# Kernel optimization log

Hardware: AMD Instinct MI355X
Metric: run time of the kernel (lower is better)

Reference implementation:

```python
import jax, jax.numpy as jnp
import numpy as np

B, S, H = 2, 1024, 2048
NH, NKV, HD = 16, 4, 128           # heads, kv heads, head_dim
E, TOPK, NG, TOPKG, M = 8, 2, 4, 2, 512  # experts, top_k, n_group, topk_group, moe ffn dim
EPS = 1e-6
THETA = 10000.0
SCALE = HD ** -0.5
RSF = 1.0  # routed_scaling_factor


def rmsnorm(x, w):
    xf = x.astype(jnp.float32)
    var = jnp.mean(xf * xf, axis=-1, keepdims=True)
    return (w * (xf * jax.lax.rsqrt(var + EPS))).astype(x.dtype)


def rotate_half(x):
    x1, x2 = jnp.split(x, 2, axis=-1)
    return jnp.concatenate([-x2, x1], axis=-1)


def setup_inputs() -> dict:
    key = jax.random.key(0)
    ks = jax.random.split(key, 16)
    s = 0.02
    hidden_states = jax.random.normal(ks[0], (B, S, H), jnp.float32)
    pos = jnp.arange(S, dtype=jnp.float32)
    inv_freq = 1.0 / (THETA ** (jnp.arange(0, HD, 2, dtype=jnp.float32) / HD))
    freqs = jnp.outer(pos, inv_freq)                       # [S, HD/2]
    emb = jnp.concatenate([freqs, freqs], axis=-1)         # [S, HD]
    cos = jnp.broadcast_to(jnp.cos(emb)[None], (B, S, HD))
    sin = jnp.broadcast_to(jnp.sin(emb)[None], (B, S, HD))
    return {
        "hidden_states": hidden_states,
        "cos": cos,
        "sin": sin,
        "ln1_w": jnp.ones((H,), jnp.float32),
        "w_qkv": jax.random.normal(ks[1], ((NH + 2 * NKV) * HD, H), jnp.float32) * s,
        "q_ln_w": jnp.ones((HD,), jnp.float32),
        "k_ln_w": jnp.ones((HD,), jnp.float32),
        "w_dense": jax.random.normal(ks[2], (H, NH * HD), jnp.float32) * s,
        "ln2_w": jnp.ones((H,), jnp.float32),
        "gate_w": jax.random.normal(ks[3], (E, H), jnp.float32) * s,
        "gate_bias": jnp.zeros((E,), jnp.float32),
        "we_gate": jax.random.normal(ks[4], (E, M, H), jnp.float32) * s,
        "we_up": jax.random.normal(ks[5], (E, M, H), jnp.float32) * s,
        "we_down": jax.random.normal(ks[6], (E, H, M), jnp.float32) * s,
        "ws_gate": jax.random.normal(ks[7], (M, H), jnp.float32) * s,
        "ws_up": jax.random.normal(ks[8], (M, H), jnp.float32) * s,
        "ws_down": jax.random.normal(ks[9], (H, M), jnp.float32) * s,
    }


def reference(hidden_states, cos, sin, ln1_w, w_qkv, q_ln_w, k_ln_w, w_dense,
              ln2_w, gate_w, gate_bias, we_gate, we_up, we_down,
              ws_gate, ws_up, ws_down):
    # ---- attention block ----
    residual = hidden_states
    x = rmsnorm(hidden_states, ln1_w)
    qkv = jnp.einsum('bsh,oh->bso', x, w_qkv).reshape(B, S, NH + 2 * NKV, HD)
    q, k, v = jnp.split(qkv, [NH, NH + NKV], axis=2)
    q = q.transpose(0, 2, 1, 3)   # [B, NH,  S, HD]
    k = k.transpose(0, 2, 1, 3)   # [B, NKV, S, HD]
    v = v.transpose(0, 2, 1, 3)
    q = rmsnorm(q, q_ln_w)
    k = rmsnorm(k, k_ln_w)
    c, sn = cos[:, None], sin[:, None]  # [B,1,S,HD]
    q = q * c + rotate_half(q) * sn
    k = k * c + rotate_half(k) * sn
    n_rep = NH // NKV
    k = jnp.repeat(k, n_rep, axis=1)
    v = jnp.repeat(v, n_rep, axis=1)
    scores = jnp.einsum('bhqd,bhkd->bhqk', q, k) * SCALE
    attn = jax.nn.softmax(scores.astype(jnp.float32), axis=-1).astype(q.dtype)
    out = jnp.einsum('bhqk,bhkd->bhqd', attn, v)
    out = out.transpose(0, 2, 1, 3).reshape(B, S, NH * HD)
    attn_out = jnp.einsum('bso,ho->bsh', out, w_dense)
    hidden = residual + attn_out

    # ---- MoE block ----
    residual = hidden
    x = rmsnorm(hidden, ln2_w).reshape(B * S, H)
    T = B * S
    logits = jnp.einsum('th,eh->te', x.astype(jnp.float32), gate_w.astype(jnp.float32))
    scores = jax.nn.sigmoid(logits)
    scores_b = scores + gate_bias
    # group-limited routing: pick topk_group groups by sum of top-2 scores per group
    gsz = E // NG
    grp = scores_b.reshape(T, NG, gsz)
    top2 = jax.lax.top_k(grp, min(2, gsz))[0].sum(-1)      # [T, NG]
    _, gidx = jax.lax.top_k(top2, TOPKG)                   # [T, TOPKG]
    gmask = jnp.zeros((T, NG), scores.dtype).at[jnp.arange(T)[:, None], gidx].set(1.0)
    emask = jnp.repeat(gmask, gsz, axis=-1)                # [T, E]
    masked = jnp.where(emask > 0, scores_b, -jnp.inf)
    _, tidx = jax.lax.top_k(masked, TOPK)                  # [T, TOPK]
    tw = jnp.take_along_axis(scores, tidx, axis=-1)
    tw = tw / (tw.sum(-1, keepdims=True) + 1e-20) * RSF
    route = jnp.zeros((T, E), x.dtype).at[jnp.arange(T)[:, None], tidx].set(tw.astype(x.dtype))
    # dense all-expert compute, combined by (sparse) routing weights
    g = jnp.einsum('th,emh->tem', x, we_gate)
    u = jnp.einsum('th,emh->tem', x, we_up)
    he = jax.nn.silu(g) * u
    oe = jnp.einsum('tem,ehm->teh', he, we_down)
    moe = jnp.einsum('te,teh->th', route, oe)
    # shared expert
    sh = jnp.einsum('th,oh->to', jax.nn.silu(x @ ws_gate.T) * (x @ ws_up.T), ws_down)
    out = residual + (moe + sh).reshape(B, S, H)
    return out
```

## Files before the change

### kernel.cpp

```cpp
#include <hip/hip_runtime.h>
#include <cstdint>
#include <cstddef>

#define T_TOK 2048
#define H_DIM 2048
#define S_LEN 1024
#define HD 128
#define NH 16
#define NKV 4
#define QKV_O 3072
#define MM 512
#define EPS 1e-6f
#define ATT_SCALE 0.08838834764831845f

typedef __bf16 bf16x8 __attribute__((ext_vector_type(8)));
typedef __bf16 bf16x4 __attribute__((ext_vector_type(4)));
typedef float  f32x4  __attribute__((ext_vector_type(4)));

__device__ __forceinline__ __bf16 f2bf(float f) {
  unsigned u = __builtin_bit_cast(unsigned, f);
  u += 0x7fffu + ((u >> 16) & 1u);
  unsigned short h = (unsigned short)(u >> 16);
  return __builtin_bit_cast(__bf16, h);
}
__device__ __forceinline__ f32x4 fzero4() {
  f32x4 z; z[0] = 0.f; z[1] = 0.f; z[2] = 0.f; z[3] = 0.f; return z;
}
__device__ __forceinline__ void gld16(const __bf16* g, __bf16* l) {
  __builtin_amdgcn_global_load_lds(
      (const __attribute__((address_space(1))) unsigned int*)g,
      (__attribute__((address_space(3))) unsigned int*)l, 16, 0, 0);
}

__global__ __launch_bounds__(256) void wconv_k(
    const float* __restrict__ s0, const float* __restrict__ s1,
    __bf16* __restrict__ dst) {
  size_t e = ((size_t)blockIdx.x * 256 + threadIdx.x) * 16;
  const size_t E0 = 6291456;
  const float* src; size_t base;
  if (e < E0) { src = s0; base = 0; }
  else        { src = s1; base = E0; }
  const float4* sp = (const float4*)(src + (e - base));
  float4 f0 = sp[0], f1 = sp[1], f2 = sp[2], f3 = sp[3];
  bf16x8 o0, o1;
  o0[0] = f2bf(f0.x); o0[1] = f2bf(f0.y); o0[2] = f2bf(f0.z); o0[3] = f2bf(f0.w);
  o0[4] = f2bf(f1.x); o0[5] = f2bf(f1.y); o0[6] = f2bf(f1.z); o0[7] = f2bf(f1.w);
  o1[0] = f2bf(f2.x); o1[1] = f2bf(f2.y); o1[2] = f2bf(f2.z); o1[3] = f2bf(f2.w);
  o1[4] = f2bf(f3.x); o1[5] = f2bf(f3.y); o1[6] = f2bf(f3.z); o1[7] = f2bf(f3.w);
  *(bf16x8*)(dst + e) = o0;
  *(bf16x8*)(dst + e + 8) = o1;
}

__global__ __launch_bounds__(256) void rmsnorm_k(const float* __restrict__ X,
                                                 const float* __restrict__ W,
                                                 __bf16* __restrict__ Y) {
  int t = blockIdx.x;
  int tid = threadIdx.x, lane = tid & 63, wid = tid >> 6;
  const float4* row = (const float4*)(X + (size_t)t * H_DIM);
  float4 v0 = row[tid], v1 = row[tid + 256];
  float ss = v0.x*v0.x + v0.y*v0.y + v0.z*v0.z + v0.w*v0.w
           + v1.x*v1.x + v1.y*v1.y + v1.z*v1.z + v1.w*v1.w;
  #pragma unroll
  for (int m = 1; m <= 32; m <<= 1) ss += __shfl_xor(ss, m, 64);
  __shared__ float red[4];
  if (lane == 0) red[wid] = ss;
  __syncthreads();
  float tot = red[0] + red[1] + red[2] + red[3];
  float sc = rsqrtf(tot * (1.f / H_DIM) + EPS);
  const float4* wp = (const float4*)W;
  float4 w0 = wp[tid], w1 = wp[tid + 256];
  bf16x4 o;
  o[0] = f2bf(v0.x*w0.x*sc); o[1] = f2bf(v0.y*w0.y*sc);
  o[2] = f2bf(v0.z*w0.z*sc); o[3] = f2bf(v0.w*w0.w*sc);
  *(bf16x4*)&Y[(size_t)t*H_DIM + tid*4] = o;
  o[0] = f2bf(v1.x*w1.x*sc); o[1] = f2bf(v1.y*w1.y*sc);
  o[2] = f2bf(v1.z*w1.z*sc); o[3] = f2bf(v1.w*w1.w*sc);
  *(bf16x4*)&Y[(size_t)t*H_DIM + 1024 + tid*4] = o;
}

template<int MODE>
__global__ __launch_bounds__(256) void gemm64_nt(
    const __bf16* __restrict__ A, const __bf16* __restrict__ B,
    float* __restrict__ C, __bf16* __restrict__ OB,
    const float* __restrict__ resid, int N, int K) {
  int m0 = blockIdx.y * 64;
  int n0 = blockIdx.x * 128;
  __shared__ __bf16 sA[2][64 * 64];
  __shared__ __bf16 sB[2][128 * 64];
  int tid = threadIdx.x, lane = tid & 63, wid = tid >> 6;
  int quad = lane >> 4, l16 = lane & 15;
  int wm = wid & 1, wn = wid >> 1;

  const __bf16* gA[2]; const __bf16* gB[4];
  #pragma unroll
  for (int i = 0; i < 2; i++) {
    int p = tid + 256 * i;
    int row = p >> 3, sc = p & 7, gc = sc ^ (row & 7);
    gA[i] = A + (size_t)(m0 + row) * K + gc * 8;
  }
  #pragma unroll
  for (int i = 0; i < 4; i++) {
    int p = tid + 256 * i;
    int row = p >> 3, sc = p & 7, gc = sc ^ (row & 7);
    gB[i] = B + (size_t)(n0 + row) * K + gc * 8;
  }
  f32x4 acc[2][4];
  #pragma unroll
  for (int i = 0; i < 2; i++)
    #pragma unroll
    for (int j = 0; j < 4; j++) acc[i][j] = fzero4();

  auto stage = [&](int buf, int k0) {
    #pragma unroll
    for (int i = 0; i < 2; i++)
      gld16(gA[i] + k0, &sA[buf][(tid + 256 * i) * 8]);
    #pragma unroll
    for (int i = 0; i < 4; i++)
      gld16(gB[i] + k0, &sB[buf][(tid + 256 * i) * 8]);
  };
  stage(0, 0);
  int cur = 0;
  for (int k0 = 0; k0 < K; k0 += 64) {
    __syncthreads();
    if (k0 + 64 < K) stage(cur ^ 1, k0 + 64);
    #pragma unroll
    for (int ks = 0; ks < 64; ks += 32) {
      int cb = ks >> 3;
      bf16x8 aF[2], bF[4];
      #pragma unroll
      for (int mt = 0; mt < 2; mt++) {
        int row = wm * 32 + mt * 16 + l16;
        int pos = row * 8 + ((cb + quad) ^ (row & 7));
        aF[mt] = *(const bf16x8*)&sA[cur][pos * 8];
      }
      #pragma unroll
      for (int nt = 0; nt < 4; nt++) {
        int row = wn * 64 + nt * 16 + l16;
        int pos = row * 8 + ((cb + quad) ^ (row & 7));
        bF[nt] = *(const bf16x8*)&sB[cur][pos * 8];
      }
      #pragma unroll
      for (int mt = 0; mt < 2; mt++)
        #pragma unroll
        for (int nt = 0; nt < 4; nt++)
          acc[mt][nt] = __builtin_amdgcn_mfma_f32_16x16x32_bf16(
              aF[mt], bF[nt], acc[mt][nt], 0, 0, 0);
    }
    cur ^= 1;
  }
  #pragma unroll
  for (int mt = 0; mt < 2; mt++) {
    #pragma unroll
    for (int nt = 0; nt < 4; nt++) {
      #pragma unroll
      for (int r = 0; r < 4; r++) {
        int grow = m0 + wm*32 + mt*16 + quad*4 + r;
        int gcol = n0 + wn*64 + nt*16 + l16;
        float val = acc[mt][nt][r];
        if (MODE == 0) {
          OB[(size_t)grow * N + gcol] = f2bf(val);
        } else {
          C[(size_t)grow * H_DIM + gcol] = val + resid[(size_t)grow * H_DIM + gcol];
        }
      }
    }
  }
}

__global__ __launch_bounds__(256) void gemm_down(
    const __bf16* __restrict__ A, const float* __restrict__ B,
    const float* __restrict__ B2, __bf16* __restrict__ OB,
    const int* __restrict__ list, const signed char* __restrict__ jsl,
    const int* __restrict__ cnt) {
  int e  = blockIdx.z;
  int ne = (e == 8) ? T_TOK : cnt[e];
  int m0 = blockIdx.y * 128;
  if (m0 >= ne) return;
  int n0 = blockIdx.x * 128;
  const __bf16* Ab = A + (size_t)e * T_TOK * MM;
  const float*  Bb = (e < 8) ? B + (size_t)e * H_DIM * MM : B2;
  const int K = MM;
  __shared__ __bf16 sA[2][128 * 64];
  __shared__ __bf16 sB[2][128 * 64];
  int tid = threadIdx.x, lane = tid & 63, wid = tid >> 6;
  int quad = lane >> 4, l16 = lane & 15;
  int wm = wid & 1, wn = wid >> 1;

  const __bf16* gA[4]; const float* gB[4];
  #pragma unroll
  for (int i = 0; i < 4; i++) {
    int p = tid + 256 * i;
    int row = p >> 3, sc = p & 7, gc = sc ^ (row & 7);
    gA[i] = Ab + (size_t)(m0 + row) * K + gc * 8;
    gB[i] = Bb + (size_t)(n0 + row) * K + gc * 8;
  }
  f32x4 acc[4][4];
  #pragma unroll
  for (int i = 0; i < 4; i++)
    #pragma unroll
    for (int j = 0; j < 4; j++) acc[i][j] = fzero4();

  f32x4 br[4][2];
  auto stageA = [&](int buf, int k0) {
    #pragma unroll
    for (int i = 0; i < 4; i++)
      gld16(gA[i] + k0, &sA[buf][(tid + 256 * i) * 8]);
  };
  auto loadB = [&](int k0) {
    #pragma unroll
    for (int i = 0; i < 4; i++) {
      br[i][0] = *(const f32x4*)(gB[i] + k0);
      br[i][1] = *(const f32x4*)(gB[i] + k0 + 4);
    }
  };
  auto writeB = [&](int buf) {
    #pragma unroll
    for (int i = 0; i < 4; i++) {
      int p = tid + 256 * i;
      bf16x8 o;
      #pragma unroll
      for (int j = 0; j < 4; j++) { o[j] = f2bf(br[i][0][j]); o[j+4] = f2bf(br[i][1][j]); }
      *(bf16x8*)&sB[buf][p * 8] = o;
    }
  };
  stageA(0, 0); loadB(0); writeB(0);
  int cur = 0;
  for (int k0 = 0; k0 < K; k0 += 64) {
    __syncthreads();
    bool nxt = (k0 + 64 < K);
    if (nxt) { stageA(cur ^ 1, k0 + 64); loadB(k0 + 64); }
    #pragma unroll
    for (int ks = 0; ks < 64; ks += 32) {
      int cb = ks >> 3;
      bf16x8 aF[4], bF[4];
      #pragma unroll
      for (int mt = 0; mt < 4; mt++) {
        int row = wm * 64 + mt * 16 + l16;
        int pos = row * 8 + ((cb + quad) ^ (row & 7));
        aF[mt] = *(const bf16x8*)&sA[cur][pos * 8];
      }
      #pragma unroll
      for (int nt = 0; nt < 4; nt++) {
        int row = wn * 64 + nt * 16 + l16;
        int pos = row * 8 + ((cb + quad) ^ (row & 7));
        bF[nt] = *(const bf16x8*)&sB[cur][pos * 8];
      }
      #pragma unroll
      for (int mt = 0; mt < 4; mt++)
        #pragma unroll
        for (int nt = 0; nt < 4; nt++)
          acc[mt][nt] = __builtin_amdgcn_mfma_f32_16x16x32_bf16(
              aF[mt], bF[nt], acc[mt][nt], 0, 0, 0);
    }
    if (nxt) writeB(cur ^ 1);
    cur ^= 1;
  }
  #pragma unroll
  for (int mt = 0; mt < 4; mt++) {
    #pragma unroll
    for (int nt = 0; nt < 4; nt++) {
      #pragma unroll
      for (int r = 0; r < 4; r++) {
        int grow = m0 + wm*64 + mt*16 + quad*4 + r;
        int gcol = n0 + wn*64 + nt*16 + l16;
        if (grow < ne) {
          int tk = list[e * T_TOK + grow];
          int j  = (e == 8) ? 2 : (int)jsl[e * T_TOK + grow];
          OB[((size_t)tk * 3 + j) * H_DIM + gcol] = f2bf(acc[mt][nt][r]);
        }
      }
    }
  }
}

__global__ __launch_bounds__(256) void combine_k(const __bf16* __restrict__ buf,
                                                 float* __restrict__ out) {
  int t = blockIdx.x, tid = threadIdx.x;
  const __bf16* base = buf + (size_t)t * 3 * H_DIM;
  bf16x8 v0 = *(const bf16x8*)(base + tid * 8);
  bf16x8 v1 = *(const bf16x8*)(base + H_DIM + tid * 8);
  bf16x8 v2 = *(const bf16x8*)(base + 2 * H_DIM + tid * 8);
  float* o = out + (size_t)t * H_DIM + tid * 8;
  float4 a = *(float4*)o, b = *(float4*)(o + 4);
  a.x += (float)v0[0] + (float)v1[0] + (float)v2[0];
  a.y += (float)v0[1] + (float)v1[1] + (float)v2[1];
  a.z += (float)v0[2] + (float)v1[2] + (float)v2[2];
  a.w += (float)v0[3] + (float)v1[3] + (float)v2[3];
  b.x += (float)v0[4] + (float)v1[4] + (float)v2[4];
  b.y += (float)v0[5] + (float)v1[5] + (float)v2[5];
  b.z += (float)v0[6] + (float)v1[6] + (float)v2[6];
  b.w += (float)v0[7] + (float)v1[7] + (float)v2[7];
  *(float4*)o = a; *(float4*)(o + 4) = b;
}

__global__ __launch_bounds__(256) void rope_k(
    const __bf16* __restrict__ qkv, const float* __restrict__ qlw,
    const float* __restrict__ klw, const float* __restrict__ cosp,
    const float* __restrict__ sinp, __bf16* __restrict__ qb,
    __bf16* __restrict__ kb, __bf16* __restrict__ vb) {
  int bid = blockIdx.x;
  int t = bid / 6;
  int head = (bid % 6) * 4 + (threadIdx.x >> 6);
  int b = t >> 10, s = t & 1023;
  int d = threadIdx.x & 63;
  const __bf16* src = qkv + (size_t)t * QKV_O + head * HD;
  float x1 = (float)src[d], x2 = (float)src[d + 64];
  if (head < 20) {
    float ssq = x1*x1 + x2*x2;
    #pragma unroll
    for (int m = 1; m <= 32; m <<= 1) ssq += __shfl_xor(ssq, m, 64);
    float sc = rsqrtf(ssq * (1.f / HD) + EPS);
    const float* w = (head < 16) ? qlw : klw;
    x1 = x1 * sc * w[d];
    x2 = x2 * sc * w[d + 64];
    size_t cb = (size_t)t * HD;
    float c1 = cosp[cb + d], s1 = sinp[cb + d];
    float c2 = cosp[cb + d + 64], s2 = sinp[cb + d + 64];
    float o1 = x1 * c1 - x2 * s1;
    float o2 = x2 * c2 + x1 * s2;
    if (head < 16) {
      __bf16* dst = qb + (((size_t)(b * NH + head)) * S_LEN + s) * HD;
      dst[d] = f2bf(o1); dst[d + 64] = f2bf(o2);
    } else {
      int kv = head - 16;
      __bf16* dst = kb + (((size_t)(b * NKV + kv)) * S_LEN + s) * HD;
      dst[d] = f2bf(o1); dst[d + 64] = f2bf(o2);
    }
  } else {
    int kv = head - 20;
    __bf16* dst = vb + (((size_t)(b * NKV + kv)) * S_LEN + s) * HD;
    dst[d] = src[d]; dst[d + 64] = src[d + 64];
  }
}

__global__ __launch_bounds__(256) void vtrans_k(const __bf16* __restrict__ vb,
                                                __bf16* __restrict__ vt) {
  int s0 = blockIdx.x * 64, d0 = blockIdx.y * 64, g = blockIdx.z;
  __shared__ __bf16 sT[64 * 80];
  int tid = threadIdx.x;
  const __bf16* src = vb + (size_t)g * S_LEN * HD;
  #pragma unroll
  for (int i = 0; i < 2; i++) {
    int p = tid + 256 * i;
    int rs = p >> 3, cc = p & 7;
    bf16x8 v = *(const bf16x8*)(src + (size_t)(s0 + rs) * HD + d0 + cc * 8);
    #pragma unroll
    for (int j = 0; j < 8; j++) sT[(cc * 8 + j) * 80 + rs] = v[j];
  }
  __syncthreads();
  __bf16* dst = vt + (size_t)g * HD * S_LEN;
  #pragma unroll
  for (int i = 0; i < 2; i++) {
    int p = tid + 256 * i;
    int rd = p >> 3, cs = p & 7;
    bf16x8 v = *(const bf16x8*)&sT[rd * 80 + cs * 8];
    *(bf16x8*)(dst + (size_t)(d0 + rd) * S_LEN + s0 + cs * 8) = v;
  }
}

__global__ __launch_bounds__(256) void flash_k(
    const __bf16* __restrict__ qb, const __bf16* __restrict__ kb,
    const __bf16* __restrict__ vt, __bf16* __restrict__ outb) {
  int qt = blockIdx.x, bh = blockIdx.y;
  int b = bh >> 4, h = bh & 15, kv = h >> 2;
  int tid = threadIdx.x, lane = tid & 63, wid = tid >> 6;
  int quad = lane >> 4, l16 = lane & 15;
  __shared__ __bf16 sQ[64 * 128];
  __shared__ __bf16 sKP[64 * 128];
  __shared__ __bf16 sVt[128 * 64];
  __bf16* sK = sKP;
  __bf16* sP = sKP;

  const __bf16* qsrc = qb + (((size_t)(b * NH + h)) * S_LEN + qt * 64) * HD;
  #pragma unroll
  for (int i = 0; i < 4; i++) {
    int p = tid + 256 * i;
    int row = p >> 4, sc = p & 15, gc = sc ^ (row & 7);
    gld16(qsrc + (size_t)row * HD + gc * 8, &sQ[p * 8]);
  }
  const __bf16* kbase  = kb + ((size_t)(b * NKV + kv)) * S_LEN * HD;
  const __bf16* vtbase = vt + ((size_t)(b * NKV + kv)) * HD * S_LEN;
  const __bf16* gK[4]; const __bf16* gV[4];
  #pragma unroll
  for (int i = 0; i < 4; i++) {
    int p = tid + 256 * i;
    int rowk = p >> 4, sck = p & 15, gck = sck ^ (rowk & 7);
    gK[i] = kbase + (size_t)rowk * HD + gck * 8;
    int rowv = p >> 3, scv = p & 7, gcv = scv ^ (rowv & 7);
    gV[i] = vtbase + (size_t)rowv * S_LEN + gcv * 8;
  }
  float mrow[4], lrow[4];
  #pragma unroll
  for (int r = 0; r < 4; r++) { mrow[r] = -__builtin_inff(); lrow[r] = 0.f; }
  f32x4 accO[8];
  #pragma unroll
  for (int i = 0; i < 8; i++) accO[i] = fzero4();

  for (int kt = 0; kt < 16; kt++) {
    __syncthreads();
    #pragma unroll
    for (int i = 0; i < 4; i++) {
      gld16(gK[i] + (size_t)kt * 64 * HD, &sK[(tid + 256 * i) * 8]);
      gld16(gV[i] + kt * 64, &sVt[(tid + 256 * i) * 8]);
    }
    __syncthreads();
    f32x4 accS[4];
    #pragma unroll
    for (int jt = 0; jt < 4; jt++) accS[jt] = fzero4();
    int rowA = wid * 16 + l16;
    #pragma unroll
    for (int ks2 = 0; ks2 < 4; ks2++) {
      int posA = rowA * 16 + ((ks2 * 4 + quad) ^ (rowA & 7));
      bf16x8 aF = *(const bf16x8*)&sQ[posA * 8];
      #pragma unroll
      for (int jt = 0; jt < 4; jt++) {
        int rowB = jt * 16 + l16;
        int posB = rowB * 16 + ((ks2 * 4 + quad) ^ (rowB & 7));
        bf16x8 bF = *(const bf16x8*)&sK[posB * 8];
        accS[jt] = __builtin_amdgcn_mfma_f32_16x16x32_bf16(aF, bF, accS[jt], 0, 0, 0);
      }
    }
    float alpha[4];
    #pragma unroll
    for (int r = 0; r < 4; r++) {
      float mx = -__builtin_inff();
      #pragma unroll
      for (int jt = 0; jt < 4; jt++) {
        accS[jt][r] *= ATT_SCALE;
        mx = fmaxf(mx, accS[jt][r]);
      }
      #pragma unroll
      for (int m = 1; m <= 8; m <<= 1) mx = fmaxf(mx, __shfl_xor(mx, m, 64));
      float mn = fmaxf(mrow[r], mx);
      float al = __expf(mrow[r] - mn);
      float rs = 0.f;
      #pragma unroll
      for (int jt = 0; jt < 4; jt++) {
        float p = __expf(accS[jt][r] - mn);
        accS[jt][r] = p;
        rs += p;
      }
      #pragma unroll
      for (int m = 1; m <= 8; m <<= 1) rs += __shfl_xor(rs, m, 64);
      lrow[r] = lrow[r] * al + rs;
      mrow[r] = mn;
      alpha[r] = al;
    }
    #pragma unroll
    for (int nt = 0; nt < 8; nt++)
      #pragma unroll
      for (int r = 0; r < 4; r++) accO[nt][r] *= alpha[r];
    __syncthreads();
    #pragma unroll
    for (int jt = 0; jt < 4; jt++)
      #pragma unroll
      for (int r = 0; r < 4; r++)
        sP[(wid * 16 + quad * 4 + r) * 72 + jt * 16 + l16] = f2bf(accS[jt][r]);
    __syncthreads();
    #pragma unroll
    for (int ks2 = 0; ks2 < 2; ks2++) {
      bf16x8 aF = *(const bf16x8*)&sP[(wid * 16 + l16) * 72 + ks2 * 32 + quad * 8];
      #pragma unroll
      for (int nt = 0; nt < 8; nt++) {
        int rowB = nt * 16 + l16;
        int posB = rowB * 8 + ((ks2 * 4 + quad) ^ (rowB & 7));
        bf16x8 bF = *(const bf16x8*)&sVt[posB * 8];
        accO[nt] = __builtin_amdgcn_mfma_f32_16x16x32_bf16(aF, bF, accO[nt], 0, 0, 0);
      }
    }
  }
  #pragma unroll
  for (int nt = 0; nt < 8; nt++) {
    #pragma unroll
    for (int r = 0; r < 4; r++) {
      int srow = qt * 64 + wid * 16 + quad * 4 + r;
      float val = accO[nt][r] / lrow[r];
      outb[((size_t)(b * S_LEN + srow)) * H_DIM + h * HD + nt * 16 + l16] = f2bf(val);
    }
  }
}

__global__ __launch_bounds__(256) void router_k(
    const float* __restrict__ hid, const float* __restrict__ ln2w,
    const float* __restrict__ gw, const float* __restrict__ gb,
    int* __restrict__ cnt, int* __restrict__ list, float* __restrict__ wsl,
    signed char* __restrict__ jsl) {
  int t = blockIdx.x;
  int tid = threadIdx.x, lane = tid & 63, wid = tid >> 6;
  const float4* row = (const float4*)(hid + (size_t)t * H_DIM);
  float4 v0 = row[tid], v1 = row[tid + 256];
  float ss = v0.x*v0.x + v0.y*v0.y + v0.z*v0.z + v0.w*v0.w
           + v1.x*v1.x + v1.y*v1.y + v1.z*v1.z + v1.w*v1.w;
  #pragma unroll
  for (int m = 1; m <= 32; m <<= 1) ss += __shfl_xor(ss, m, 64);
  __shared__ float red[4];
  __shared__ float lred[4][8];
  if (lane == 0) red[wid] = ss;
  __syncthreads();
  float tot = red[0] + red[1] + red[2] + red[3];
  float sc = rsqrtf(tot * (1.f / H_DIM) + EPS);
  const float4* wp = (const float4*)ln2w;
  float4 w0 = wp[tid], w1 = wp[tid + 256];
  float x0 = v0.x*w0.x*sc, x1 = v0.y*w0.y*sc, x2 = v0.z*w0.z*sc, x3 = v0.w*w0.w*sc;
  float x4 = v1.x*w1.x*sc, x5 = v1.y*w1.y*sc, x6 = v1.z*w1.z*sc, x7 = v1.w*w1.w*sc;
  float pe[8];
  #pragma unroll
  for (int e = 0; e < 8; e++) {
    const float4* gp = (const float4*)(gw + (size_t)e * H_DIM);
    float4 g0 = gp[tid], g1 = gp[tid + 256];
    float d = x0*g0.x + x1*g0.y + x2*g0.z + x3*g0.w
            + x4*g1.x + x5*g1.y + x6*g1.z + x7*g1.w;
    #pragma unroll
    for (int m = 1; m <= 32; m <<= 1) d += __shfl_xor(d, m, 64);
    pe[e] = d;
  }
  if (lane == 0) {
    #pragma unroll
    for (int e = 0; e < 8; e++) lred[wid][e] = pe[e];
  }
  __syncthreads();
  if (tid == 0) {
    float s[8], sb[8];
    #pragma unroll
    for (int e = 0; e < 8; e++) {
      float lg = lred[0][e] + lred[1][e] + lred[2][e] + lred[3][e];
      s[e] = 1.f / (1.f + __expf(-lg));
      sb[e] = s[e] + gb[e];
    }
    float gs[4];
    #pragma unroll
    for (int g = 0; g < 4; g++) gs[g] = sb[2 * g] + sb[2 * g + 1];
    int g1 = 0;
    for (int g = 1; g < 4; g++) if (gs[g] > gs[g1]) g1 = g;
    int g2 = -1;
    for (int g = 0; g < 4; g++) if (g != g1 && (g2 < 0 || gs[g] > gs[g2])) g2 = g;
    unsigned emask = (3u << (2 * g1)) | (3u << (2 * g2));
    int e1 = -1;
    for (int e = 0; e < 8; e++) if (((emask >> e) & 1u) && (e1 < 0 || sb[e] > sb[e1])) e1 = e;
    int e2 = -1;
    for (int e = 0; e < 8; e++) if (((emask >> e) & 1u) && e != e1 && (e2 < 0 || sb[e] > sb[e2])) e2 = e;
    float w1s = s[e1], w2s = s[e2];
    float dn = w1s + w2s + 1e-20f;
    w1s /= dn; w2s /= dn;
    int p1 = atomicAdd(&cnt[e1], 1);
    list[e1 * T_TOK + p1] = t; wsl[e1 * T_TOK + p1] = w1s; jsl[e1 * T_TOK + p1] = 0;
    int p2 = atomicAdd(&cnt[e2], 1);
    list[e2 * T_TOK + p2] = t; wsl[e2 * T_TOK + p2] = w2s; jsl[e2 * T_TOK + p2] = 1;
    list[8 * T_TOK + t] = t; wsl[8 * T_TOK + t] = 1.f;
  }
}

__global__ __launch_bounds__(256) void gemm_gateup(
    const __bf16* __restrict__ X, const float* __restrict__ weg,
    const float* __restrict__ weu, const float* __restrict__ wsg,
    const float* __restrict__ wsu, const int* __restrict__ list,
    const float* __restrict__ wsl, const int* __restrict__ cnt,
    __bf16* __restrict__ he) {
  int e = blockIdx.z;
  int ne = (e == 8) ? T_TOK : cnt[e];
  int m0 = blockIdx.y * 128;
  if (m0 >= ne) return;
  int n0 = blockIdx.x * 64;
  const float* bg = (e < 8) ? weg + (size_t)e * MM * H_DIM : wsg;
  const float* bu = (e < 8) ? weu + (size_t)e * MM * H_DIM : wsu;
  const int* lst = list + e * T_TOK;
  __shared__ __bf16 sA[2][128 * 64];
  __shared__ __bf16 sBg[2][64 * 64];
  __shared__ __bf16 sBu[2][64 * 64];
  int tid = threadIdx.x, lane = tid & 63, wid = tid >> 6;
  int quad = lane >> 4, l16 = lane & 15;

  const __bf16* gA[4]; const float* gBg[2]; const float* gBu[2];
  #pragma unroll
  for (int i = 0; i < 4; i++) {
    int p = tid + 256 * i;
    int row = p >> 3, sc = p & 7, gc = sc ^ (row & 7);
    int r = m0 + row; if (r >= ne) r = ne - 1;
    int tk = lst[r];
    gA[i] = X + (size_t)tk * H_DIM + gc * 8;
  }
  #pragma unroll
  for (int i = 0; i < 2; i++) {
    int p = tid + 256 * i;
    int row = p >> 3, sc = p & 7, gc = sc ^ (row & 7);
    gBg[i] = bg + (size_t)(n0 + row) * H_DIM + gc * 8;
    gBu[i] = bu + (size_t)(n0 + row) * H_DIM + gc * 8;
  }
  f32x4 ag[2][4], au[2][4];
  #pragma unroll
  for (int i = 0; i < 2; i++)
    #pragma unroll
    for (int j = 0; j < 4; j++) { ag[i][j] = fzero4(); au[i][j] = fzero4(); }

  f32x4 bgr[2][2], bur[2][2];
  auto stageA = [&](int buf, int k0) {
    #pragma unroll
    for (int i = 0; i < 4; i++)
      gld16(gA[i] + k0, &sA[buf][(tid + 256 * i) * 8]);
  };
  auto loadB = [&](int k0) {
    #pragma unroll
    for (int i = 0; i < 2; i++) {
      bgr[i][0] = *(const f32x4*)(gBg[i] + k0);
      bgr[i][1] = *(const f32x4*)(gBg[i] + k0 + 4);
      bur[i][0] = *(const f32x4*)(gBu[i] + k0);
      bur[i][1] = *(const f32x4*)(gBu[i] + k0 + 4);
    }
  };
  auto writeB = [&](int buf) {
    #pragma unroll
    for (int i = 0; i < 2; i++) {
      int p = tid + 256 * i;
      bf16x8 og, ou;
      #pragma unroll
      for (int j = 0; j < 4; j++) {
        og[j] = f2bf(bgr[i][0][j]); og[j+4] = f2bf(bgr[i][1][j]);
        ou[j] = f2bf(bur[i][0][j]); ou[j+4] = f2bf(bur[i][1][j]);
      }
      *(bf16x8*)&sBg[buf][p * 8] = og;
      *(bf16x8*)&sBu[buf][p * 8] = ou;
    }
  };
  stageA(0, 0); loadB(0); writeB(0);
  int cur = 0;
  for (int k0 = 0; k0 < H_DIM; k0 += 64) {
    __syncthreads();
    bool nxt = (k0 + 64 < H_DIM);
    if (nxt) { stageA(cur ^ 1, k0 + 64); loadB(k0 + 64); }
    #pragma unroll
    for (int ks = 0; ks < 64; ks += 32) {
      int cb = ks >> 3;
      bf16x8 aF[2], gF[4], uF[4];
      #pragma unroll
      for (int mt = 0; mt < 2; mt++) {
        int row = wid * 32 + mt * 16 + l16;
        int pos = row * 8 + ((cb + quad) ^ (row & 7));
        aF[mt] = *(const bf16x8*)&sA[cur][pos * 8];
      }
      #pragma unroll
      for (int nt = 0; nt < 4; nt++) {
        int row = nt * 16 + l16;
        int pos = row * 8 + ((cb + quad) ^ (row & 7));
        gF[nt] = *(const bf16x8*)&sBg[cur][pos * 8];
        uF[nt] = *(const bf16x8*)&sBu[cur][pos * 8];
      }
      #pragma unroll
      for (int mt = 0; mt < 2; mt++)
        #pragma unroll
        for (int nt = 0; nt < 4; nt++) {
          ag[mt][nt] = __builtin_amdgcn_mfma_f32_16x16x32_bf16(aF[mt], gF[nt], ag[mt][nt], 0, 0, 0);
          au[mt][nt] = __builtin_amdgcn_mfma_f32_16x16x32_bf16(aF[mt], uF[nt], au[mt][nt], 0, 0, 0);
        }
    }
    if (nxt) writeB(cur ^ 1);
    cur ^= 1;
  }
  #pragma unroll
  for (int mt = 0; mt < 2; mt++) {
    #pragma unroll
    for (int nt = 0; nt < 4; nt++) {
      #pragma unroll
      for (int r = 0; r < 4; r++) {
        int row_l = wid * 32 + mt * 16 + quad * 4 + r;
        int grow = m0 + row_l;
        if (grow < ne) {
          float g = ag[mt][nt][r], u = au[mt][nt][r];
          float hv = g / (1.f + __expf(-g)) * u;
          hv *= wsl[e * T_TOK + grow];
          he[((size_t)e * T_TOK + grow) * MM + n0 + nt * 16 + l16] = f2bf(hv);
        }
      }
    }
  }
}

extern "C" void kernel_launch(void* const* d_in, const int* in_sizes, int n_in,
                              void* d_out, int out_size, void* d_ws, size_t ws_size,
                              hipStream_t stream) {
  (void)in_sizes; (void)n_in; (void)out_size; (void)ws_size;
  const float* hs     = (const float*)d_in[0];
  const float* cosp   = (const float*)d_in[1];
  const float* sinp   = (const float*)d_in[2];
  const float* ln1w   = (const float*)d_in[3];
  const float* wqkv   = (const float*)d_in[4];
  const float* qlw    = (const float*)d_in[5];
  const float* klw    = (const float*)d_in[6];
  const float* wdense = (const float*)d_in[7];
  const float* ln2w   = (const float*)d_in[8];
  const float* gw     = (const float*)d_in[9];
  const float* gbias  = (const float*)d_in[10];
  const float* weg    = (const float*)d_in[11];
  const float* weu    = (const float*)d_in[12];
  const float* wed    = (const float*)d_in[13];
  const float* wsg    = (const float*)d_in[14];
  const float* wsu    = (const float*)d_in[15];
  const float* wsd    = (const float*)d_in[16];
  float* out = (float*)d_out;

  char* ws = (char*)d_ws;
  size_t off = 0;
  auto alloc = [&](size_t b) { char* p = ws + off; off += (b + 255) & ~(size_t)255; return p; };
  __bf16* wbf   = (__bf16*)alloc((size_t)10485760 * 2);
  __bf16* xb1   = (__bf16*)alloc((size_t)T_TOK * H_DIM * 2);
  __bf16* qreg  = (__bf16*)alloc((size_t)T_TOK * 3 * H_DIM * 2);
  __bf16* qb    = (__bf16*)alloc((size_t)2 * NH  * S_LEN * HD * 2);
  __bf16* kb    = (__bf16*)alloc((size_t)2 * NKV * S_LEN * HD * 2);
  __bf16* vb    = (__bf16*)alloc((size_t)2 * NKV * S_LEN * HD * 2);
  __bf16* vt    = (__bf16*)alloc((size_t)2 * NKV * S_LEN * HD * 2);
  __bf16* outb  = (__bf16*)alloc((size_t)T_TOK * H_DIM * 2);
  __bf16* xb2   = (__bf16*)alloc((size_t)T_TOK * H_DIM * 2);
  int*    cnt   = (int*)   alloc(256);
  int*    list  = (int*)   alloc((size_t)9 * T_TOK * 4);
  float*  wsl   = (float*) alloc((size_t)9 * T_TOK * 4);
  signed char* jsl = (signed char*)alloc((size_t)9 * T_TOK);
  __bf16* qkvb  = qreg;
  __bf16* buf   = qreg;
  __bf16* he    = qb;

  const __bf16* wqkv_bf   = wbf;
  const __bf16* wdense_bf = wbf + 6291456;

  hipMemsetAsync(cnt, 0, 256, stream);
  wconv_k<<<2560, 256, 0, stream>>>(wqkv, wdense, wbf);
  rmsnorm_k<<<T_TOK, 256, 0, stream>>>(hs, ln1w, xb1);
  gemm64_nt<0><<<dim3(QKV_O / 128, T_TOK / 64), 256, 0, stream>>>(
      xb1, wqkv_bf, nullptr, qkvb, nullptr, QKV_O, H_DIM);
  rope_k<<<T_TOK * 6, 256, 0, stream>>>(qkvb, qlw, klw, cosp, sinp, qb, kb, vb);
  vtrans_k<<<dim3(16, 2, 8), 256, 0, stream>>>(vb, vt);
  flash_k<<<dim3(S_LEN / 64, 2 * NH), 256, 0, stream>>>(qb, kb, vt, outb);
  gemm64_nt<1><<<dim3(H_DIM / 128, T_TOK / 64), 256, 0, stream>>>(
      outb, wdense_bf, out, nullptr, hs, H_DIM, H_DIM);
  rmsnorm_k<<<T_TOK, 256, 0, stream>>>(out, ln2w, xb2);
  router_k<<<T_TOK, 256, 0, stream>>>(out, ln2w, gw, gbias, cnt, list, wsl, jsl);
  gemm_gateup<<<dim3(MM / 64, T_TOK / 128, 9), 256, 0, stream>>>(
      xb2, weg, weu, wsg, wsu, list, wsl, cnt, he);
  gemm_down<<<dim3(H_DIM / 128, T_TOK / 128, 9), 256, 0, stream>>>(
      he, wed, wsd, buf, list, jsl, cnt);
  combine_k<<<T_TOK, 256, 0, stream>>>(buf, out);
}
```

Baseline: 508.6 us.

## Deepen B-operand register prefetch in MoE GEMMs and narrow down-proj N tile

Both MoE GEMMs now keep two register sets of fp32 weight slices in flight, loaded two K-steps ahead, with the main loop unrolled by two over the shared-memory double buffer. This is meant to hide global load latency for the fp32 weights, which are converted to bf16 before the shared-memory write. gemm_down also moves from 128x128 to 128x64 tiles, with each wave owning 32 rows and all 64 columns. That doubles the block count and cuts accumulator registers, at the cost of more prefetch registers and more re-reads of the A operand.

After: 518.1 us. About the same (+1.9%).

```diff
diff --git a/kernel.cpp b/kernel.cpp
--- a/kernel.cpp
+++ b/kernel.cpp
@@ -176,93 +176,122 @@
   int ne = (e == 8) ? T_TOK : cnt[e];
   int m0 = blockIdx.y * 128;
   if (m0 >= ne) return;
-  int n0 = blockIdx.x * 128;
+  int n0 = blockIdx.x * 64;
   const __bf16* Ab = A + (size_t)e * T_TOK * MM;
   const float*  Bb = (e < 8) ? B + (size_t)e * H_DIM * MM : B2;
   const int K = MM;
   __shared__ __bf16 sA[2][128 * 64];
-  __shared__ __bf16 sB[2][128 * 64];
+  __shared__ __bf16 sB[2][64 * 64];
   int tid = threadIdx.x, lane = tid & 63, wid = tid >> 6;
   int quad = lane >> 4, l16 = lane & 15;
-  int wm = wid & 1, wn = wid >> 1;
-
-  const __bf16* gA[4]; const float* gB[4];
+
+  const __bf16* gA[4]; const float* gB[2];
   #pragma unroll
   for (int i = 0; i < 4; i++) {
     int p = tid + 256 * i;
     int row = p >> 3, sc = p & 7, gc = sc ^ (row & 7);
     gA[i] = Ab + (size_t)(m0 + row) * K + gc * 8;
+  }
+  #pragma unroll
+  for (int i = 0; i < 2; i++) {
+    int p = tid + 256 * i;
+    int row = p >> 3, sc = p & 7, gc = sc ^ (row & 7);
     gB[i] = Bb + (size_t)(n0 + row) * K + gc * 8;
   }
-  f32x4 acc[4][4];
-  #pragma unroll
-  for (int i = 0; i < 4; i++)
+  f32x4 acc[2][4];
+  #pragma unroll
+  for (int i = 0; i < 2; i++)
     #pragma unroll
     for (int j = 0; j < 4; j++) acc[i][j] = fzero4();
 
-  f32x4 br[4][2];
+  f32x4 s0[2][2], s1[2][2];
   auto stageA = [&](int buf, int k0) {
     #pragma unroll
     for (int i = 0; i < 4; i++)
       gld16(gA[i] + k0, &sA[buf][(tid + 256 * i) * 8]);
   };
-  auto loadB = [&](int k0) {
-    #pragma unroll
-    for (int i = 0; i < 4; i++) {
-      br[i][0] = *(const f32x4*)(gB[i] + k0);
-      br[i][1] = *(const f32x4*)(gB[i] + k0 + 4);
-    }
-  };
-  auto writeB = [&](int buf) {
-    #pragma unroll
-    for (int i = 0; i < 4; i++) {
+  auto loadB0 = [&](int k0) {
+    #pragma unroll
+    for (int i = 0; i < 2; i++) {
+      s0[i][0] = *(const f32x4*)(gB[i] + k0);
+      s0[i][1] = *(const f32x4*)(gB[i] + k0 + 4);
+    }
+  };
+  auto loadB1 = [&](int k0) {
+    #pragma unroll
+    for (int i = 0; i < 2; i++) {
+      s1[i][0] = *(const f32x4*)(gB[i] + k0);
+      s1[i][1] = *(const f32x4*)(gB[i] + k0 + 4);
+    }
+  };
+  auto writeB0 = [&](int buf) {
+    #pragma unroll
+    for (int i = 0; i < 2; i++) {
       int p = tid + 256 * i;
       bf16x8 o;
       #pragma unroll
-      for (int j = 0; j < 4; j++) { o[j] = f2bf(br[i][0][j]); o[j+4] = f2bf(br[i][1][j]); }
+      for (int j = 0; j < 4; j++) { o[j] = f2bf(s0[i][0][j]); o[j+4] = f2bf(s0[i][1][j]); }
       *(bf16x8*)&sB[buf][p * 8] = o;
     }
   };
-  stageA(0, 0); loadB(0); writeB(0);
-  int cur = 0;
-  for (int k0 = 0; k0 < K; k0 += 64) {
-    __syncthreads();
-    bool nxt = (k0 + 64 < K);
-    if (nxt) { stageA(cur ^ 1, k0 + 64); loadB(k0 + 64); }
+  auto writeB1 = [&](int buf) {
+    #pragma unroll
+    for (int i = 0; i < 2; i++) {
+      int p = tid + 256 * i;
+      bf16x8 o;
+      #pragma unroll
+      for (int j = 0; j < 4; j++) { o[j] = f2bf(s1[i][0][j]); o[j+4] = f2bf(s1[i][1][j]); }
+      *(bf16x8*)&sB[buf][p * 8] = o;
+    }
+  };
+  auto compute = [&](int cur) {
     #pragma unroll
     for (int ks = 0; ks < 64; ks += 32) {
       int cb = ks >> 3;
-      bf16x8 aF[4], bF[4];
-      #pragma unroll
-      for (int mt = 0; mt < 4; mt++) {
-        int row = wm * 64 + mt * 16 + l16;
+      bf16x8 aF[2], bF[4];
+      #pragma unroll
+      for (int mt = 0; mt < 2; mt++) {
+        int row = wid * 32 + mt * 16 + l16;
         int pos = row * 8 + ((cb + quad) ^ (row & 7));
         aF[mt] = *(const bf16x8*)&sA[cur][pos * 8];
       }
       #pragma unroll
       for (int nt = 0; nt < 4; nt++) {
-        int row = wn * 64 + nt * 16 + l16;
+        int row = nt * 16 + l16;
         int pos = row * 8 + ((cb + quad) ^ (row & 7));
         bF[nt] = *(const bf16x8*)&sB[cur][pos * 8];
       }
       #pragma unroll
-      for (int mt = 0; mt < 4; mt++)
+      for (int mt = 0; mt < 2; mt++)
         #pragma unroll
         for (int nt = 0; nt < 4; nt++)
           acc[mt][nt] = __builtin_amdgcn_mfma_f32_16x16x32_bf16(
               aF[mt], bF[nt], acc[mt][nt], 0, 0, 0);
     }
-    if (nxt) writeB(cur ^ 1);
-    cur ^= 1;
-  }
-  #pragma unroll
-  for (int mt = 0; mt < 4; mt++) {
+  };
+  loadB0(0); writeB0(0); loadB0(64); loadB1(128); stageA(0, 0);
+  for (int k0 = 0; k0 < K; k0 += 128) {
+    __syncthreads();
+    stageA(1, k0 + 64);
+    writeB0(1);
+    if (k0 + 192 < K) loadB0(k0 + 192);
+    compute(0);
+    __syncthreads();
+    if (k0 + 128 < K) {
+      stageA(0, k0 + 128);
+      writeB1(0);
+      if (k0 + 256 < K) loadB1(k0 + 256);
+    }
+    compute(1);
+  }
+  #pragma unroll
+  for (int mt = 0; mt < 2; mt++) {
     #pragma unroll
     for (int nt = 0; nt < 4; nt++) {
       #pragma unroll
       for (int r = 0; r < 4; r++) {
-        int grow = m0 + wm*64 + mt*16 + quad*4 + r;
-        int gcol = n0 + wn*64 + nt*16 + l16;
+        int grow = m0 + wid*32 + mt*16 + quad*4 + r;
+        int gcol = n0 + nt*16 + l16;
         if (grow < ne) {
           int tk = list[e * T_TOK + grow];
           int j  = (e == 8) ? 2 : (int)jsl[e * T_TOK + grow];
@@ -592,41 +621,59 @@
     #pragma unroll
     for (int j = 0; j < 4; j++) { ag[i][j] = fzero4(); au[i][j] = fzero4(); }
 
-  f32x4 bgr[2][2], bur[2][2];
+  f32x4 g0r[2][2], u0r[2][2], g1r[2][2], u1r[2][2];
   auto stageA = [&](int buf, int k0) {
     #pragma unroll
     for (int i = 0; i < 4; i++)
       gld16(gA[i] + k0, &sA[buf][(tid + 256 * i) * 8]);
   };
-  auto loadB = [&](int k0) {
+  auto loadB0 = [&](int k0) {
     #pragma unroll
     for (int i = 0; i < 2; i++) {
-      bgr[i][0] = *(const f32x4*)(gBg[i] + k0);
-      bgr[i][1] = *(const f32x4*)(gBg[i] + k0 + 4);
-      bur[i][0] = *(const f32x4*)(gBu[i] + k0);
-      bur[i][1] = *(const f32x4*)(gBu[i] + k0 + 4);
-    }
-  };
-  auto writeB = [&](int buf) {
+      g0r[i][0] = *(const f32x4*)(gBg[i] + k0);
+      g0r[i][1] = *(const f32x4*)(gBg[i] + k0 + 4);
+      u0r[i][0] = *(const f32x4*)(gBu[i] + k0);
+      u0r[i][1] = *(const f32x4*)(gBu[i] + k0 + 4);
+    }
+  };
+  auto loadB1 = [&](int k0) {
+    #pragma unroll
+    for (int i = 0; i < 2; i++) {
+      g1r[i][0] = *(const f32x4*)(gBg[i] + k0);
+      g1r[i][1] = *(const f32x4*)(gBg[i] + k0 + 4);
+      u1r[i][0] = *(const f32x4*)(gBu[i] + k0);
+      u1r[i][1] = *(const f32x4*)(gBu[i] + k0 + 4);
+    }
+  };
+  auto writeB0 = [&](int buf) {
     #pragma unroll
     for (int i = 0; i < 2; i++) {
       int p = tid + 256 * i;
       bf16x8 og, ou;
       #pragma unroll
       for (int j = 0; j < 4; j++) {
-        og[j] = f2bf(bgr[i][0][j]); og[j+4] = f2bf(bgr[i][1][j]);
-        ou[j] = f2bf(bur[i][0][j]); ou[j+4] = f2bf(bur[i][1][j]);
+        og[j] = f2bf(g0r[i][0][j]); og[j+4] = f2bf(g0r[i][1][j]);
+        ou[j] = f2bf(u0r[i][0][j]); ou[j+4] = f2bf(u0r[i][1][j]);
       }
       *(bf16x8*)&sBg[buf][p * 8] = og;
       *(bf16x8*)&sBu[buf][p * 8] = ou;
     }
   };
-  stageA(0, 0); loadB(0); writeB(0);
-  int cur = 0;
-  for (int k0 = 0; k0 < H_DIM; k0 += 64) {
-    __syncthreads();
-    bool nxt = (k0 + 64 < H_DIM);
-    if (nxt) { stageA(cur ^ 1, k0 + 64); loadB(k0 + 64); }
+  auto writeB1 = [&](int buf) {
+    #pragma unroll
+    for (int i = 0; i < 2; i++) {
+      int p = tid + 256 * i;
+      bf16x8 og, ou;
+      #pragma unroll
+      for (int j = 0; j < 4; j++) {
+        og[j] = f2bf(g1r[i][0][j]); og[j+4] = f2bf(g1r[i][1][j]);
+        ou[j] = f2bf(u1r[i][0][j]); ou[j+4] = f2bf(u1r[i][1][j]);
+      }
+      *(bf16x8*)&sBg[buf][p * 8] = og;
+      *(bf16x8*)&sBu[buf][p * 8] = ou;
+    }
+  };
+  auto compute = [&](int cur) {
     #pragma unroll
     for (int ks = 0; ks < 64; ks += 32) {
       int cb = ks >> 3;
@@ -652,8 +699,21 @@
           au[mt][nt] = __builtin_amdgcn_mfma_f32_16x16x32_bf16(aF[mt], uF[nt], au[mt][nt], 0, 0, 0);
         }
     }
-    if (nxt) writeB(cur ^ 1);
-    cur ^= 1;
+  };
+  loadB0(0); writeB0(0); loadB0(64); loadB1(128); stageA(0, 0);
+  for (int k0 = 0; k0 < H_DIM; k0 += 128) {
+    __syncthreads();
+    stageA(1, k0 + 64);
+    writeB0(1);
+    if (k0 + 192 < H_DIM) loadB0(k0 + 192);
+    compute(0);
+    __syncthreads();
+    if (k0 + 128 < H_DIM) {
+      stageA(0, k0 + 128);
+      writeB1(0);
+      if (k0 + 256 < H_DIM) loadB1(k0 + 256);
+    }
+    compute(1);
   }
   #pragma unroll
   for (int mt = 0; mt < 2; mt++) {
@@ -734,7 +794,7 @@
   router_k<<<T_TOK, 256, 0, stream>>>(out, ln2w, gw, gbias, cnt, list, wsl, jsl);
   gemm_gateup<<<dim3(MM / 64, T_TOK / 128, 9), 256, 0, stream>>>(
       xb2, weg, weu, wsg, wsu, list, wsl, cnt, he);
-  gemm_down<<<dim3(H_DIM / 128, T_TOK / 128, 9), 256, 0, stream>>>(
+  gemm_down<<<dim3(H_DIM / 64, T_TOK / 128, 9), 256, 0, stream>>>(
       he, wed, wsd, buf, list, jsl, cnt);
   combine_k<<<T_TOK, 256, 0, stream>>>(buf, out);
 }
```
